# Kernel tuning notes

Measured on AMD Instinct MI355X. Metric: run time of the kernel, lower is better.

The kernel has to match this reference:

```python
import jax, jax.numpy as jnp
import numpy as np
from jax import lax

B, L, D_MODEL = 2, 1024, 2048
D_INNER, D_STATE, D_CONV, DT_RANK = 4096, 16, 4, 128
EPS = 1e-5


def setup_inputs() -> dict:
    key = jax.random.key(0)
    ks = jax.random.split(key, 10)
    sc = lambda k, shape, s=0.02: jax.random.normal(k, shape, jnp.float32) * s
    # A initialized like real Mamba: A_log = log(arange(1, d_state+1))
    A_log = jnp.log(jnp.broadcast_to(jnp.arange(1, D_STATE + 1, dtype=jnp.float32), (D_INNER, D_STATE)))
    return {
        "hidden_states": jax.random.normal(ks[0], (B, L, D_MODEL), jnp.float32),
        "residual": jax.random.normal(ks[1], (B, L, D_MODEL), jnp.float32),
        "norm_weight": jnp.ones((D_MODEL,), jnp.float32),
        "in_proj_w": sc(ks[2], (2 * D_INNER, D_MODEL)),
        "conv_w": sc(ks[3], (D_INNER, D_CONV), 0.1),
        "conv_b": jnp.zeros((D_INNER,), jnp.float32),
        "x_proj_w": sc(ks[4], (DT_RANK + 2 * D_STATE, D_INNER)),
        "dt_proj_w": sc(ks[5], (D_INNER, DT_RANK), 0.1),
        "dt_proj_b": sc(ks[6], (D_INNER,), 0.5),
        "A_log": A_log,
        "D_param": jnp.ones((D_INNER,), jnp.float32),
        "out_proj_w": sc(ks[7], (D_MODEL, D_INNER)),
    }


def _rmsnorm(x, w, eps=EPS):
    var = jnp.mean(jnp.square(x), axis=-1, keepdims=True)
    return x * lax.rsqrt(var + eps) * w


def _mamba_block(hidden_states, residual, norm_weight, in_proj_w, conv_w, conv_b,
                 x_proj_w, dt_proj_w, dt_proj_b, A_log, D_param, out_proj_w):
    # fused add + RMSNorm, residual kept in fp32 (prenorm=True)
    residual = (hidden_states + residual).astype(jnp.float32)
    hs = _rmsnorm(residual, norm_weight)

    # ---- Mamba mixer ----
    xz = jnp.einsum("bld,ed->ble", hs, in_proj_w)          # [B,L,2*d_inner]
    x, z = jnp.split(xz, 2, axis=-1)                        # each [B,L,d_inner]

    # depthwise causal conv over time
    xt = x.swapaxes(1, 2)                                   # [B,d_inner,L]
    xt = lax.conv_general_dilated(
        xt, conv_w[:, None, :], window_strides=(1,), padding=[(D_CONV - 1, 0)],
        dimension_numbers=("NCH", "OIH", "NCH"), feature_group_count=D_INNER)
    xt = xt + conv_b[:, None]
    x = jax.nn.silu(xt).swapaxes(1, 2)                      # [B,L,d_inner]

    # input-dependent dt, B, C
    x_dbl = jnp.einsum("bld,ed->ble", x, x_proj_w)          # [B,L,dt_rank+2*d_state]
    dt, Bm, Cm = jnp.split(x_dbl, [DT_RANK, DT_RANK + D_STATE], axis=-1)
    dt = jax.nn.softplus(jnp.einsum("blr,dr->bld", dt, dt_proj_w) + dt_proj_b)  # [B,L,d_inner]

    A = -jnp.exp(A_log)                                     # [d_inner,d_state]

    # selective scan: h_t = exp(dt_t*A) h_{t-1} + dt_t*B_t*x_t ; y_t = <h_t, C_t>
    def step(h, inp):
        dt_t, x_t, B_t, C_t = inp                           # [B,di],[B,di],[B,ds],[B,ds]
        dA = jnp.exp(dt_t[:, :, None] * A)                  # [B,di,ds]
        h = dA * h + (dt_t * x_t)[:, :, None] * B_t[:, None, :]
        y = jnp.einsum("bds,bs->bd", h, C_t)
        return h, y

    xs = (dt.swapaxes(0, 1), x.swapaxes(0, 1), Bm.swapaxes(0, 1), Cm.swapaxes(0, 1))
    h0 = jnp.zeros((B, D_INNER, D_STATE), jnp.float32)
    _, ys = lax.scan(step, h0, xs)                          # ys: [L,B,d_inner]
    y = ys.swapaxes(0, 1) + x * D_param                     # [B,L,d_inner]

    y = y * jax.nn.silu(z)
    out = jnp.einsum("bld,ed->ble", y, out_proj_w)          # [B,L,d_model]
    return out, residual


def reference(hidden_states, residual, norm_weight, in_proj_w, conv_w, conv_b,
              x_proj_w, dt_proj_w, dt_proj_b, A_log, D_param, out_proj_w):
    return _mamba_block(hidden_states, residual, norm_weight, in_proj_w, conv_w,
                        conv_b, x_proj_w, dt_proj_w, dt_proj_b, A_log, D_param,
                        out_proj_w)
```

## Files before the change

kernel.cpp:

```cpp
#include <hip/hip_runtime.h>
#include <hip/hip_bf16.h>
#include <math.h>

#define B_SZ    2
#define L_SZ    1024
#define DMODEL  2048
#define DINNER  4096
#define DSTATE  16
#define DCONV   4
#define DTRANK  128
#define NROWS   (B_SZ * L_SZ)
#define NCHUNK  16
#define CHUNKLEN (L_SZ / NCHUNK)

typedef __hip_bfloat16 bf16;
typedef __attribute__((ext_vector_type(8))) short  short8;
typedef __attribute__((ext_vector_type(4))) float  floatx4;

static __device__ __forceinline__ float b2f(bf16 v) { return __bfloat162float(v); }
static __device__ __forceinline__ bf16  f2b(float v) { return __float2bfloat16(v); }
static __device__ __forceinline__ short f2bs(float v) {
    return (short)__builtin_bit_cast(unsigned short, __float2bfloat16(v));
}

static __device__ __forceinline__ void cvt8(const short8 v, float* out) {
    #pragma unroll
    for (int i = 0; i < 8; i++) {
        unsigned int u = ((unsigned int)(unsigned short)v[i]) << 16;
        out[i] = __builtin_bit_cast(float, u);
    }
}

static __device__ __forceinline__ float softplus_safe(float x) {
    return fmaxf(x, 0.f) + log1pf(__expf(-fabsf(x)));
}

static __device__ __forceinline__ void gload_lds16(const bf16* g, bf16* l) {
    __builtin_amdgcn_global_load_lds(
        (const __attribute__((address_space(1))) void*)g,
        (__attribute__((address_space(3))) void*)l,
        16, 0, 0);
}


__global__ void probe_kernel(const void* nw, int* flag) {
    if (threadIdx.x == 0 && blockIdx.x == 0) {
        const unsigned short* p = (const unsigned short*)nw;
        *flag = (p[0] == 0x3F80u) ? 0 : 1;
    }
}
__global__ void assert_fp32_kernel(const int* flag, float* out) {
    if (*flag == 0) out[blockIdx.x * 256 + threadIdx.x] = 888.0f;
}
__global__ void fill_diag_kernel(unsigned short* out, int n) {
    int i = blockIdx.x * 256 + threadIdx.x;
    if (i < n) out[i] = 0x4442;
}

__global__ __launch_bounds__(256) void cvt_w_kernel(
    const float* __restrict__ in, bf16* __restrict__ out, int n)
{
    int i = (blockIdx.x * 256 + threadIdx.x) * 8;
    if (i < n) {
        float4 a = *(const float4*)(in + i);
        float4 b = *(const float4*)(in + i + 4);
        short8 o;
        o[0] = f2bs(a.x); o[1] = f2bs(a.y); o[2] = f2bs(a.z); o[3] = f2bs(a.w);
        o[4] = f2bs(b.x); o[5] = f2bs(b.y); o[6] = f2bs(b.z); o[7] = f2bs(b.w);
        *(short8*)(out + i) = o;
    }
}

__global__ __launch_bounds__(256) void addnorm_kernel(
    const float* __restrict__ h, const float* __restrict__ r,
    const float* __restrict__ w, bf16* __restrict__ hs_out)
{
    const int row = blockIdx.x;
    const int t   = threadIdx.x;
    const size_t base = (size_t)row * DMODEL;

    float vals[8];
    float ss = 0.f;
    #pragma unroll
    for (int i = 0; i < 8; i++) {
        int c = t + i * 256;
        float v = h[base + c] + r[base + c];
        vals[i] = v;
        ss += v * v;
    }
    #pragma unroll
    for (int off = 32; off > 0; off >>= 1) ss += __shfl_down(ss, off);
    __shared__ float wsum[4];
    if ((t & 63) == 0) wsum[t >> 6] = ss;
    __syncthreads();
    float tot = wsum[0] + wsum[1] + wsum[2] + wsum[3];
    float scale = rsqrtf(tot / (float)DMODEL + 1e-5f);

    #pragma unroll
    for (int i = 0; i < 8; i++) {
        int c = t + i * 256;
        hs_out[base + c] = f2b(vals[i] * scale * w[c]);
    }
}

__global__ __launch_bounds__(256) void residual_out_kernel(
    const float* __restrict__ h, const float* __restrict__ r,
    float* __restrict__ resp)
{
    int i = (blockIdx.x * 256 + threadIdx.x) * 4;
    float4 a = *(const float4*)(h + i);
    float4 b = *(const float4*)(r + i);
    float4 o = {a.x + b.x, a.y + b.y, a.z + b.z, a.w + b.w};
    *(float4*)(resp + i) = o;
}

__global__ __launch_bounds__(256) void addf_kernel(
    float* __restrict__ outp, const float* __restrict__ c1)
{
    int i = (blockIdx.x * 256 + threadIdx.x) * 4;
    float4 a = *(const float4*)(outp + i);
    float4 b = *(const float4*)(c1 + i);
    float4 o = {a.x + b.x, a.y + b.y, a.z + b.z, a.w + b.w};
    *(float4*)(outp + i) = o;
}

__global__ __launch_bounds__(512, 2) void gemm_bigtile(
    const bf16* __restrict__ A, const bf16* __restrict__ B,
    bf16* __restrict__ C, int N, int K, int lda, int ldb, int ldc)
{
    __shared__ bf16 sA[4][8192];
    __shared__ bf16 sB[4][8192];

    const int t     = threadIdx.x;
    const int lane  = t & 63;
    const int w     = t >> 6;
    const int wm    = w & 1;
    const int wn    = w >> 1;
    const int idx16 = lane & 15;
    const int quad  = lane >> 4;

    const int tilesN = N >> 8;
    const int bid    = blockIdx.x;
    const int m_blk  = (bid / tilesN) << 8;
    const int n_blk  = (bid % tilesN) << 8;

    const int srow  = t >> 2;
    const int sslot = t & 3;
    const int gswz  = ((sslot ^ ((srow >> 1) & 3)) << 3);
    const bf16* gA = A + (size_t)(m_blk + srow) * lda + gswz;
    const bf16* gB = B + (size_t)(n_blk + srow) * ldb + gswz;

    bf16* ldsA = &sA[0][0] + (w << 9);
    bf16* ldsB = &sB[0][0] + (w << 9);

    const int rswz = ((quad ^ ((idx16 >> 1) & 3)) << 3);
    const int aoff = ((wm << 7) + idx16) * 32 + rswz;
    const int boff = ((wn << 6) + idx16) * 32 + rswz;

#define STAGE_A(tt) do { const int _r = (tt) & 3; const size_t _k = (size_t)(tt) << 5; \
    gload_lds16(gA + _k,                      ldsA + _r * 8192); \
    gload_lds16(gA + ((size_t)lda << 7) + _k, ldsA + _r * 8192 + 4096); } while (0)
#define STAGE_B(tt) do { const int _r = (tt) & 3; const size_t _k = (size_t)(tt) << 5; \
    gload_lds16(gB + _k,                      ldsB + _r * 8192); \
    gload_lds16(gB + ((size_t)ldb << 7) + _k, ldsB + _r * 8192 + 4096); } while (0)

    floatx4 acc[8][4] = {};
    const int NT = K >> 5;

    STAGE_A(0); STAGE_B(0);
    STAGE_A(1); STAGE_B(1);
    STAGE_A(2); STAGE_B(2);
    asm volatile("s_waitcnt vmcnt(8)" ::: "memory");
    __builtin_amdgcn_s_barrier();
    __builtin_amdgcn_sched_barrier(0);

    #pragma unroll 1
    for (int tt = 0; tt < NT; ++tt) {
        const bf16* la = &sA[tt & 3][0] + aoff;
        const bf16* lb = &sB[tt & 3][0] + boff;

        short8 af[4], bfr[4];
        #pragma unroll
        for (int i = 0; i < 4; i++) af[i]  = *(const short8*)(la + i * 512);
        #pragma unroll
        for (int j = 0; j < 4; j++) bfr[j] = *(const short8*)(lb + j * 512);
        if (tt + 3 < NT) STAGE_A(tt + 3);
        asm volatile("s_waitcnt lgkmcnt(0)" ::: "memory");
        __builtin_amdgcn_sched_barrier(0);
        __builtin_amdgcn_s_setprio(1);
        #pragma unroll
        for (int i = 0; i < 4; i++)
            #pragma unroll
            for (int j = 0; j < 4; j++)
                acc[i][j] = __builtin_amdgcn_mfma_f32_16x16x32_bf16(
                    af[i], bfr[j], acc[i][j], 0, 0, 0);
        __builtin_amdgcn_s_setprio(0);

        short8 ag[4];
        #pragma unroll
        for (int i = 0; i < 4; i++) ag[i] = *(const short8*)(la + (i + 4) * 512);
        if (tt + 3 < NT) STAGE_B(tt + 3);
        asm volatile("s_waitcnt lgkmcnt(0)" ::: "memory");
        __builtin_amdgcn_sched_barrier(0);
        __builtin_amdgcn_s_setprio(1);
        #pragma unroll
        for (int i = 0; i < 4; i++)
            #pragma unroll
            for (int j = 0; j < 4; j++)
                acc[i + 4][j] = __builtin_amdgcn_mfma_f32_16x16x32_bf16(
                    ag[i], bfr[j], acc[i + 4][j], 0, 0, 0);
        __builtin_amdgcn_s_setprio(0);

        const int ahead = NT - 1 - tt;
        if (ahead >= 3)      asm volatile("s_waitcnt vmcnt(8)" ::: "memory");
        else if (ahead == 2) asm volatile("s_waitcnt vmcnt(4)" ::: "memory");
        else if (ahead == 1) asm volatile("s_waitcnt vmcnt(0)" ::: "memory");
        if (ahead > 0) {
            __builtin_amdgcn_s_barrier();
            __builtin_amdgcn_sched_barrier(0);
        }
    }
#undef STAGE_A
#undef STAGE_B

    #pragma unroll
    for (int i = 0; i < 8; i++) {
        #pragma unroll
        for (int j = 0; j < 4; j++) {
            const int r0 = m_blk + (wm << 7) + i * 16 + quad * 4;
            const int c  = n_blk + (wn << 6) + j * 16 + idx16;
            #pragma unroll
            for (int rr = 0; rr < 4; rr++)
                C[(size_t)(r0 + rr) * ldc + c] = f2b(acc[i][j][rr]);
        }
    }
}

__global__ __launch_bounds__(256) void gemm_lds_sk2(
    const bf16* __restrict__ A, const bf16* __restrict__ B,
    float* __restrict__ C0, float* __restrict__ C1)
{
    __shared__ bf16 As[128 * 32];
    __shared__ bf16 Bs[128 * 32];

    const int t    = threadIdx.x;
    const int lane = t & 63;
    const int wave = t >> 6;
    const int ks   = blockIdx.x >> 8;
    const int bid  = blockIdx.x & 255;
    const int m_blk = (bid >> 4) * 128;
    const int n_blk = (bid & 15) * 128;
    const int kbase = ks * 2048;

    const int idx16 = lane & 15;
    const int quad  = lane >> 4;
    const int wm = (wave & 1) * 64;
    const int wn = (wave >> 1) * 64;

    const int row_s = t >> 2;
    const int koff  = ((t & 3) ^ ((row_s >> 1) & 3)) * 8;
    const bf16* gA = A + (size_t)(m_blk + row_s) * 4096 + koff + kbase;
    const bf16* gB = B + (size_t)(n_blk + row_s) * 4096 + koff + kbase;
    bf16* lA = As + wave * 512;
    bf16* lB = Bs + wave * 512;

    const int rswz = (quad ^ ((idx16 >> 1) & 3)) * 8;

    floatx4 acc[4][4] = {};

    for (int k0 = 0; k0 < 2048; k0 += 32) {
        gload_lds16(gA + k0,                    lA);
        gload_lds16(gA + (size_t)64 * 4096 + k0, lA + 2048);
        gload_lds16(gB + k0,                    lB);
        gload_lds16(gB + (size_t)64 * 4096 + k0, lB + 2048);
        __syncthreads();

        short8 af[4], bfr[4];
        #pragma unroll
        for (int i = 0; i < 4; i++)
            af[i]  = *(const short8*)(As + (wm + i * 16 + idx16) * 32 + rswz);
        #pragma unroll
        for (int j = 0; j < 4; j++)
            bfr[j] = *(const short8*)(Bs + (wn + j * 16 + idx16) * 32 + rswz);
        #pragma unroll
        for (int i = 0; i < 4; i++)
            #pragma unroll
            for (int j = 0; j < 4; j++)
                acc[i][j] = __builtin_amdgcn_mfma_f32_16x16x32_bf16(
                    af[i], bfr[j], acc[i][j], 0, 0, 0);
        __syncthreads();
    }

    float* C = ks ? C1 : C0;
    #pragma unroll
    for (int i = 0; i < 4; i++) {
        #pragma unroll
        for (int j = 0; j < 4; j++) {
            const int r0 = m_blk + wm + i * 16 + quad * 4;
            const int c  = n_blk + wn + j * 16 + idx16;
            #pragma unroll
            for (int r = 0; r < 4; r++)
                C[(size_t)(r0 + r) * DMODEL + c] = acc[i][j][r];
        }
    }
}

__global__ __launch_bounds__(256) void gemm_g2_sk(
    const bf16* __restrict__ x, const bf16* __restrict__ W,
    float* __restrict__ part)
{
    const int lane = threadIdx.x & 63;
    const int gw   = blockIdx.x * 4 + (threadIdx.x >> 6);
    const int tile = gw >> 2;
    const int s    = gw & 3;
    const int wm = tile / 10;
    const int wn = tile % 10;
    const int idx16 = lane & 15, quad = lane >> 4;
    const int k0 = s * 1024;

    floatx4 acc = {};
    const bf16* Ap = x + (size_t)(wm * 16 + idx16) * DINNER + quad * 8 + k0;
    const bf16* Bp = W + (size_t)(wn * 16 + idx16) * DINNER + quad * 8 + k0;
    for (int k = 0; k < 1024; k += 32) {
        short8 af  = *(const short8*)(Ap + k);
        short8 bfr = *(const short8*)(Bp + k);
        acc = __builtin_amdgcn_mfma_f32_16x16x32_bf16(af, bfr, acc, 0, 0, 0);
    }
    #pragma unroll
    for (int r = 0; r < 4; r++)
        part[((size_t)s * NROWS + wm * 16 + quad * 4 + r) * 160 + wn * 16 + idx16]
            = acc[r];
}

__global__ __launch_bounds__(256) void g2_reduce_kernel(
    const float* __restrict__ part, bf16* __restrict__ xdbl)
{
    int i = blockIdx.x * 256 + threadIdx.x;
    float v = part[i] + part[327680 + i] + part[2 * 327680 + i]
            + part[3 * 327680 + i];
    xdbl[i] = f2b(v);
}

__global__ __launch_bounds__(256) void gemm_g3_direct(
    const bf16* __restrict__ xdbl, const bf16* __restrict__ W,
    const float* __restrict__ bias, bf16* __restrict__ dtout)
{
    const int lane = threadIdx.x & 63;
    const int gw   = blockIdx.x * 4 + (threadIdx.x >> 6);
    const int wm = gw >> 8;
    const int wn = gw & 255;
    const int idx16 = lane & 15, quad = lane >> 4;

    floatx4 acc = {};
    const bf16* Ap = xdbl + (size_t)(wm * 16 + idx16) * 160 + quad * 8;
    const bf16* Bp = W + (size_t)(wn * 16 + idx16) * DTRANK + quad * 8;
    #pragma unroll
    for (int k = 0; k < 128; k += 32) {
        short8 af  = *(const short8*)(Ap + k);
        short8 bfr = *(const short8*)(Bp + k);
        acc = __builtin_amdgcn_mfma_f32_16x16x32_bf16(af, bfr, acc, 0, 0, 0);
    }
    const int c = wn * 16 + idx16;
    const float bv = bias[c];
    #pragma unroll
    for (int r = 0; r < 4; r++)
        dtout[(size_t)(wm * 16 + quad * 4 + r) * (2 * DINNER) + c]
            = f2b(softplus_safe(acc[r] + bv));
}

__global__ __launch_bounds__(256) void conv_silu_kernel(
    const bf16* __restrict__ xz, const float* __restrict__ cw,
    const float* __restrict__ cb, bf16* __restrict__ xout)
{
    const int idx = (blockIdx.x * 256 + threadIdx.x) * 8;
    const int d0 = idx & (DINNER - 1);
    const int bl = idx >> 12;
    const int l  = bl & (L_SZ - 1);
    const int b  = bl >> 10;

    float acc[8];
    {
        float4 c0 = *(const float4*)(cb + d0);
        float4 c1 = *(const float4*)(cb + d0 + 4);
        acc[0] = c0.x; acc[1] = c0.y; acc[2] = c0.z; acc[3] = c0.w;
        acc[4] = c1.x; acc[5] = c1.y; acc[6] = c1.z; acc[7] = c1.w;
    }
    floatx4 cwv[8];
    #pragma unroll
    for (int i = 0; i < 8; i++)
        cwv[i] = *(const floatx4*)(cw + (size_t)(d0 + i) * DCONV);

    #pragma unroll
    for (int t = 0; t < DCONV; t++) {
        int ls = l - (DCONV - 1) + t;
        if (ls >= 0) {
            short8 v = *(const short8*)(xz + ((size_t)(b * L_SZ + ls)) * (2 * DINNER) + d0);
            float xf[8]; cvt8(v, xf);
            #pragma unroll
            for (int i = 0; i < 8; i++) acc[i] += cwv[i][t] * xf[i];
        }
    }
    short8 o;
    #pragma unroll
    for (int i = 0; i < 8; i++) {
        float s = acc[i] / (1.f + __expf(-acc[i]));
        o[i] = f2bs(s);
    }
    *(short8*)(xout + idx) = o;
}

__global__ __launch_bounds__(256) void scan_part1(
    const bf16* __restrict__ xz, const bf16* __restrict__ x,
    const bf16* __restrict__ xdbl, const float* __restrict__ A_log,
    float* __restrict__ hpart, float* __restrict__ dtsum)
{
    __shared__ float sBC[64 * 32];
    const int tid = threadIdx.x, bid = blockIdx.x;
    const int sub = tid & 1;
    const int d   = ((bid & 31) << 7) + (tid >> 1);
    const int b   = (bid >> 5) & 1;
    const int c   = bid >> 6;
    const size_t row0 = (size_t)b * L_SZ + c * CHUNKLEN;

    {
        int r = tid >> 2, sl = tid & 3;
        short8 v = *(const short8*)(xdbl + (row0 + r) * 160 + DTRANK + sl * 8);
        float tmp[8]; cvt8(v, tmp);
        #pragma unroll
        for (int i = 0; i < 8; i++) sBC[r * 32 + sl * 8 + i] = tmp[i];
    }
    __syncthreads();

    float Aa[8];
    #pragma unroll
    for (int s = 0; s < 8; s++)
        Aa[s] = -__expf(A_log[d * DSTATE + sub * 8 + s]);

    float h[8] = {};
    float dts = 0.f;
    const floatx4* BC4 = (const floatx4*)sBC;
    const int bc0 = sub * 2;

    #pragma unroll 1
    for (int l0 = 0; l0 < CHUNKLEN; l0 += 4) {
        float dtv[4], xv[4];
        #pragma unroll
        for (int u = 0; u < 4; u++) {
            const size_t rbl = row0 + l0 + u;
            dtv[u] = b2f(xz[rbl * (2 * DINNER) + d]);
            xv[u]  = b2f(x[rbl * DINNER + d]);
        }
        #pragma unroll
        for (int u = 0; u < 4; u++) {
            const int l = l0 + u;
            floatx4 B0 = BC4[l * 8 + bc0];
            floatx4 B1 = BC4[l * 8 + bc0 + 1];
            dts += dtv[u];
            float dx = dtv[u] * xv[u];
            #pragma unroll
            for (int s = 0; s < 4; s++)
                h[s] = __expf(dtv[u] * Aa[s]) * h[s] + dx * B0[s];
            #pragma unroll
            for (int s = 0; s < 4; s++)
                h[s + 4] = __expf(dtv[u] * Aa[s + 4]) * h[s + 4] + dx * B1[s];
        }
    }
    const size_t sbase = ((size_t)((b * DINNER + d) * NCHUNK + c)) * 16 + sub * 8;
    *(floatx4*)(hpart + sbase)     = (floatx4){h[0], h[1], h[2], h[3]};
    *(floatx4*)(hpart + sbase + 4) = (floatx4){h[4], h[5], h[6], h[7]};
    if (!sub) dtsum[(b * DINNER + d) * NCHUNK + c] = dts;
}

__global__ __launch_bounds__(256) void scan_part2(
    const float* __restrict__ A_log, float* hpart,
    const float* __restrict__ dtsum)
{
    const int t = blockIdx.x * 256 + threadIdx.x;
    const int s = t & 15;
    const int d = (t >> 4) & (DINNER - 1);
    const int b = t >> 16;
    const float Aa = -__expf(A_log[d * DSTATE + s]);
    const size_t base = (size_t)(b * DINNER + d) * NCHUNK;
    float h = 0.f;
    #pragma unroll
    for (int c = 0; c < NCHUNK; c++) {
        float tmp = hpart[(base + c) * 16 + s];
        hpart[(base + c) * 16 + s] = h;
        h = __expf(Aa * dtsum[base + c]) * h + tmp;
    }
}

__global__ __launch_bounds__(256) void scan_part3(
    const bf16* __restrict__ xz, const bf16* x,
    const bf16* __restrict__ xdbl, const float* __restrict__ A_log,
    const float* __restrict__ Dp, const float* __restrict__ hpart,
    bf16* y)
{
    __shared__ float sBC[64 * 32];
    const int tid = threadIdx.x, bid = blockIdx.x;
    const int sub = tid & 1;
    const int d   = ((bid & 31) << 7) + (tid >> 1);
    const int b   = (bid >> 5) & 1;
    const int c   = bid >> 6;
    const size_t row0 = (size_t)b * L_SZ + c * CHUNKLEN;

    {
        int r = tid >> 2, sl = tid & 3;
        short8 v = *(const short8*)(xdbl + (row0 + r) * 160 + DTRANK + sl * 8);
        float tmp[8]; cvt8(v, tmp);
        #pragma unroll
        for (int i = 0; i < 8; i++) sBC[r * 32 + sl * 8 + i] = tmp[i];
    }
    __syncthreads();

    float Aa[8];
    #pragma unroll
    for (int s = 0; s < 8; s++)
        Aa[s] = -__expf(A_log[d * DSTATE + sub * 8 + s]);
    const float Dv = Dp[d];

    float h[8];
    const size_t sbase = ((size_t)((b * DINNER + d) * NCHUNK + c)) * 16 + sub * 8;
    {
        floatx4 h0 = *(const floatx4*)(hpart + sbase);
        floatx4 h1 = *(const floatx4*)(hpart + sbase + 4);
        #pragma unroll
        for (int s = 0; s < 4; s++) { h[s] = h0[s]; h[s + 4] = h1[s]; }
    }

    const floatx4* BC4 = (const floatx4*)sBC;
    const int bc0 = sub * 2;

    #pragma unroll 1
    for (int l0 = 0; l0 < CHUNKLEN; l0 += 4) {
        float dtv[4], xv[4], zv[4];
        #pragma unroll
        for (int u = 0; u < 4; u++) {
            const size_t rbl = row0 + l0 + u;
            dtv[u] = b2f(xz[rbl * (2 * DINNER) + d]);
            xv[u]  = b2f(x[rbl * DINNER + d]);
            zv[u]  = b2f(xz[rbl * (2 * DINNER) + DINNER + d]);
        }
        #pragma unroll
        for (int u = 0; u < 4; u++) {
            const int l = l0 + u;
            floatx4 B0 = BC4[l * 8 + bc0];
            floatx4 B1 = BC4[l * 8 + bc0 + 1];
            floatx4 C0 = BC4[l * 8 + 4 + bc0];
            floatx4 C1 = BC4[l * 8 + 4 + bc0 + 1];
            float dx = dtv[u] * xv[u];
            float ys = 0.f;
            #pragma unroll
            for (int s = 0; s < 4; s++) {
                h[s] = __expf(dtv[u] * Aa[s]) * h[s] + dx * B0[s];
                ys += h[s] * C0[s];
            }
            #pragma unroll
            for (int s = 0; s < 4; s++) {
                h[s + 4] = __expf(dtv[u] * Aa[s + 4]) * h[s + 4] + dx * B1[s];
                ys += h[s + 4] * C1[s];
            }
            ys += __shfl_xor(ys, 1);
            if (!sub) {
                const size_t rbl = row0 + l;
                float sig = zv[u] / (1.f + __expf(-zv[u]));
                y[rbl * DINNER + d] = f2b((ys + xv[u] * Dv) * sig);
            }
        }
    }
}

extern "C" void kernel_launch(void* const* d_in, const int* in_sizes, int n_in,
                              void* d_out, int out_size, void* d_ws, size_t ws_size,
                              hipStream_t stream)
{
    const size_t WS_NEED = 33554432ull + 16777216ull + 655360ull + 4ull;
    if (ws_size < WS_NEED) {
        fill_diag_kernel<<<(out_size + 255) / 256, 256, 0, stream>>>(
            (unsigned short*)d_out, out_size);
        return;
    }

    char* ws = (char*)d_ws;
    bf16*  xz    = (bf16*)(ws);
    float* c1    = (float*)(ws);
    bf16*  hs    = (bf16*)(ws + 33554432);
    bf16*  x     = (bf16*)(ws + 33554432);
    bf16*  y     = x;
    bf16*  xdbl  = (bf16*)(ws + 50331648);
    int*   flag  = (int*)(ws + 50987008);

    char* od = (char*)d_out;
    bf16*  w1bf  = (bf16*)od;
    bf16*  wdtbf = (bf16*)od;
    bf16*  wxbf  = (bf16*)(od + 1048576);
    float* dtsum = (float*)(od + 2359296);
    float* hpart = (float*)(od + 2883584);
    float* g2part= (float*)(od + 11272192);
    bf16*  wobf  = (bf16*)(od + 16777216);
    float* outp  = (float*)d_out;
    float* resp  = (float*)d_out + (size_t)NROWS * DMODEL;

    const float* hid = (const float*)d_in[0];
    const float* res = (const float*)d_in[1];
    const float* nw  = (const float*)d_in[2];
    const float* w1  = (const float*)d_in[3];
    const float* cw  = (const float*)d_in[4];
    const float* cb  = (const float*)d_in[5];
    const float* wx  = (const float*)d_in[6];
    const float* wdt = (const float*)d_in[7];
    const float* bdt = (const float*)d_in[8];
    const float* Al  = (const float*)d_in[9];
    const float* Dp  = (const float*)d_in[10];
    const float* wo  = (const float*)d_in[11];

    probe_kernel<<<1, 64, 0, stream>>>(d_in[2], flag);

    addnorm_kernel<<<NROWS, 256, 0, stream>>>(hid, res, nw, hs);
    cvt_w_kernel<<<(2 * DINNER * DMODEL) / 2048, 256, 0, stream>>>(
        w1, w1bf, 2 * DINNER * DMODEL);
    gemm_bigtile<<<(2048 / 256) * (8192 / 256), 512, 0, stream>>>(
        hs, w1bf, xz, 2 * DINNER, DMODEL, DMODEL, DMODEL, 2 * DINNER);

    cvt_w_kernel<<<(DINNER * DTRANK) / 2048, 256, 0, stream>>>(
        wdt, wdtbf, DINNER * DTRANK);
    cvt_w_kernel<<<(160 * DINNER) / 2048, 256, 0, stream>>>(
        wx, wxbf, 160 * DINNER);
    cvt_w_kernel<<<(DMODEL * DINNER) / 2048, 256, 0, stream>>>(
        wo, wobf, DMODEL * DINNER);

    conv_silu_kernel<<<(NROWS * DINNER) / 2048, 256, 0, stream>>>(xz, cw, cb, x);

    gemm_g2_sk<<<1280, 256, 0, stream>>>(x, wxbf, g2part);
    g2_reduce_kernel<<<(NROWS * 160) / 256, 256, 0, stream>>>(g2part, xdbl);

    gemm_g3_direct<<<8192, 256, 0, stream>>>(xdbl, wdtbf, bdt, xz);

    scan_part1<<<(NCHUNK * B_SZ * DINNER * 2) / 256, 256, 0, stream>>>(
        xz, x, xdbl, Al, hpart, dtsum);
    scan_part2<<<(B_SZ * DINNER * DSTATE) / 256, 256, 0, stream>>>(
        Al, hpart, dtsum);
    scan_part3<<<(NCHUNK * B_SZ * DINNER * 2) / 256, 256, 0, stream>>>(
        xz, x, xdbl, Al, Dp, hpart, y);

    gemm_lds_sk2<<<512, 256, 0, stream>>>(y, wobf, outp, c1);
    addf_kernel<<<(NROWS * DMODEL) / 1024, 256, 0, stream>>>(outp, c1);

    residual_out_kernel<<<(NROWS * DMODEL) / 1024, 256, 0, stream>>>(
        hid, res, resp);

    assert_fp32_kernel<<<16, 256, 0, stream>>>(flag, outp);
}
```

Measured before the change: 489.1 us.

## Pipeline out_proj split-K GEMM with 4-stage LDS ring buffer

Rewrites the out_proj split-K GEMM to use a 4-deep LDS ring buffer, issuing global-to-LDS loads three tiles ahead. Explicit vmcnt waits replace the two __syncthreads per iteration, leaving one barrier per iteration, and MFMA priority is raised while the math runs. The goal is to hide global load latency behind MFMA work. It quadruples LDS use to 64KB per block, which may limit occupancy, and relies on hand-counted waitcnt values being correct.

```diff
diff --git a/kernel.cpp b/kernel.cpp
--- a/kernel.cpp
+++ b/kernel.cpp
@@ -236,68 +236,98 @@
     }
 }
 
-__global__ __launch_bounds__(256) void gemm_lds_sk2(
+__global__ __launch_bounds__(256, 2) void gemm_sk2_r4(
     const bf16* __restrict__ A, const bf16* __restrict__ B,
     float* __restrict__ C0, float* __restrict__ C1)
 {
-    __shared__ bf16 As[128 * 32];
-    __shared__ bf16 Bs[128 * 32];
+    __shared__ bf16 sA[4][4096];
+    __shared__ bf16 sB[4][4096];
 
     const int t    = threadIdx.x;
     const int lane = t & 63;
-    const int wave = t >> 6;
+    const int w    = t >> 6;
+    const int wm   = w & 1;
+    const int wn   = w >> 1;
+    const int idx16 = lane & 15;
+    const int quad  = lane >> 4;
+
     const int ks   = blockIdx.x >> 8;
     const int bid  = blockIdx.x & 255;
     const int m_blk = (bid >> 4) * 128;
     const int n_blk = (bid & 15) * 128;
     const int kbase = ks * 2048;
 
-    const int idx16 = lane & 15;
-    const int quad  = lane >> 4;
-    const int wm = (wave & 1) * 64;
-    const int wn = (wave >> 1) * 64;
-
-    const int row_s = t >> 2;
-    const int koff  = ((t & 3) ^ ((row_s >> 1) & 3)) * 8;
-    const bf16* gA = A + (size_t)(m_blk + row_s) * 4096 + koff + kbase;
-    const bf16* gB = B + (size_t)(n_blk + row_s) * 4096 + koff + kbase;
-    bf16* lA = As + wave * 512;
-    bf16* lB = Bs + wave * 512;
-
-    const int rswz = (quad ^ ((idx16 >> 1) & 3)) * 8;
+    const int srow  = t >> 2;
+    const int sslot = t & 3;
+    const int gswz  = ((sslot ^ ((srow >> 1) & 3)) << 3);
+    const bf16* gA = A + (size_t)(m_blk + srow) * 4096 + kbase + gswz;
+    const bf16* gB = B + (size_t)(n_blk + srow) * 4096 + kbase + gswz;
+
+    bf16* ldsA = &sA[0][0] + (w << 9);
+    bf16* ldsB = &sB[0][0] + (w << 9);
+
+    const int rswz = ((quad ^ ((idx16 >> 1) & 3)) << 3);
+    const int aoff = ((wm << 6) + idx16) * 32 + rswz;
+    const int boff = ((wn << 6) + idx16) * 32 + rswz;
+
+#define STAGE_A(tt) do { const int _r = (tt) & 3; const size_t _k = (size_t)(tt) << 5; \
+    gload_lds16(gA + _k,                        ldsA + _r * 4096); \
+    gload_lds16(gA + (size_t)64 * 4096 + _k,    ldsA + _r * 4096 + 2048); } while (0)
+#define STAGE_B(tt) do { const int _r = (tt) & 3; const size_t _k = (size_t)(tt) << 5; \
+    gload_lds16(gB + _k,                        ldsB + _r * 4096); \
+    gload_lds16(gB + (size_t)64 * 4096 + _k,    ldsB + _r * 4096 + 2048); } while (0)
 
     floatx4 acc[4][4] = {};
-
-    for (int k0 = 0; k0 < 2048; k0 += 32) {
-        gload_lds16(gA + k0,                    lA);
-        gload_lds16(gA + (size_t)64 * 4096 + k0, lA + 2048);
-        gload_lds16(gB + k0,                    lB);
-        gload_lds16(gB + (size_t)64 * 4096 + k0, lB + 2048);
-        __syncthreads();
+    const int NT = 2048 >> 5;
+
+    STAGE_A(0); STAGE_B(0);
+    STAGE_A(1); STAGE_B(1);
+    STAGE_A(2); STAGE_B(2);
+    asm volatile("s_waitcnt vmcnt(8)" ::: "memory");
+    __builtin_amdgcn_s_barrier();
+    __builtin_amdgcn_sched_barrier(0);
+
+    #pragma unroll 1
+    for (int tt = 0; tt < NT; ++tt) {
+        const bf16* la = &sA[tt & 3][0] + aoff;
+        const bf16* lb = &sB[tt & 3][0] + boff;
 
         short8 af[4], bfr[4];
         #pragma unroll
-        for (int i = 0; i < 4; i++)
-            af[i]  = *(const short8*)(As + (wm + i * 16 + idx16) * 32 + rswz);
-        #pragma unroll
-        for (int j = 0; j < 4; j++)
-            bfr[j] = *(const short8*)(Bs + (wn + j * 16 + idx16) * 32 + rswz);
+        for (int i = 0; i < 4; i++) af[i]  = *(const short8*)(la + i * 512);
+        #pragma unroll
+        for (int j = 0; j < 4; j++) bfr[j] = *(const short8*)(lb + j * 512);
+        if (tt + 3 < NT) { STAGE_A(tt + 3); STAGE_B(tt + 3); }
+        asm volatile("s_waitcnt lgkmcnt(0)" ::: "memory");
+        __builtin_amdgcn_sched_barrier(0);
+        __builtin_amdgcn_s_setprio(1);
         #pragma unroll
         for (int i = 0; i < 4; i++)
             #pragma unroll
             for (int j = 0; j < 4; j++)
                 acc[i][j] = __builtin_amdgcn_mfma_f32_16x16x32_bf16(
                     af[i], bfr[j], acc[i][j], 0, 0, 0);
-        __syncthreads();
-    }
+        __builtin_amdgcn_s_setprio(0);
+
+        const int ahead = NT - 1 - tt;
+        if (ahead >= 3)      asm volatile("s_waitcnt vmcnt(8)" ::: "memory");
+        else if (ahead == 2) asm volatile("s_waitcnt vmcnt(4)" ::: "memory");
+        else if (ahead == 1) asm volatile("s_waitcnt vmcnt(0)" ::: "memory");
+        if (ahead > 0) {
+            __builtin_amdgcn_s_barrier();
+            __builtin_amdgcn_sched_barrier(0);
+        }
+    }
+#undef STAGE_A
+#undef STAGE_B
 
     float* C = ks ? C1 : C0;
     #pragma unroll
     for (int i = 0; i < 4; i++) {
         #pragma unroll
         for (int j = 0; j < 4; j++) {
-            const int r0 = m_blk + wm + i * 16 + quad * 4;
-            const int c  = n_blk + wn + j * 16 + idx16;
+            const int r0 = m_blk + (wm << 6) + i * 16 + quad * 4;
+            const int c  = n_blk + (wn << 6) + j * 16 + idx16;
             #pragma unroll
             for (int r = 0; r < 4; r++)
                 C[(size_t)(r0 + r) * DMODEL + c] = acc[i][j][r];
@@ -643,7 +673,7 @@
     scan_part3<<<(NCHUNK * B_SZ * DINNER * 2) / 256, 256, 0, stream>>>(
         xz, x, xdbl, Al, Dp, hpart, y);
 
-    gemm_lds_sk2<<<512, 256, 0, stream>>>(y, wobf, outp, c1);
+    gemm_sk2_r4<<<512, 256, 0, stream>>>(y, wobf, outp, c1);
     addf_kernel<<<(NROWS * DMODEL) / 1024, 256, 0, stream>>>(outp, c1);
 
     residual_out_kernel<<<(NROWS * DMODEL) / 1024, 256, 0, stream>>>(
```

Measured after the change: 477.7 us. -2.3%, faster.
